# Kernel optimization log

Hardware: AMD Instinct MI355X
Metric: run time of the kernel (lower is better)

Reference implementation:

```python
import jax, jax.numpy as jnp
import numpy as np

ENC, TAG, LANG, ATT = 512, 512, 512, 256
N, P = 1024, 1024


def setup_inputs() -> dict:
    key = jax.random.key(0)
    ks = jax.random.split(key, 11)
    s = lambda d: 1.0 / np.sqrt(d)
    return {
        "encoder_out": jax.random.normal(ks[0], (1, P, ENC), jnp.float32),
        "decoder_hidden": jax.random.normal(ks[1], (N, TAG), jnp.float32),
        "language_out": jax.random.normal(ks[2], (N, LANG), jnp.float32),
        "We": jax.random.uniform(ks[3], (ATT, ENC), jnp.float32, -s(ENC), s(ENC)),
        "be": jax.random.uniform(ks[4], (ATT,), jnp.float32, -s(ENC), s(ENC)),
        "Wt": jax.random.uniform(ks[5], (ATT, TAG), jnp.float32, -s(TAG), s(TAG)),
        "bt": jax.random.uniform(ks[6], (ATT,), jnp.float32, -s(TAG), s(TAG)),
        "Wl": jax.random.uniform(ks[7], (ATT, LANG), jnp.float32, -s(LANG), s(LANG)),
        "bl": jax.random.uniform(ks[8], (ATT,), jnp.float32, -s(LANG), s(LANG)),
        "Wf": jax.random.uniform(ks[9], (1, ATT), jnp.float32, -s(ATT), s(ATT)),
        "bf": jax.random.uniform(ks[10], (1,), jnp.float32, -s(ATT), s(ATT)),
    }


def reference(encoder_out, decoder_hidden, language_out, We, be, Wt, bt, Wl, bl, Wf, bf):
    # att1: (1, P, A); att2, att3: (N, A)
    att1 = jnp.einsum("bpe,ae->bpa", encoder_out, We) + be
    att2 = decoder_hidden @ Wt.T + bt
    att3 = language_out @ Wl.T + bl
    # broadcast add -> (N, P, A), relu, reduce to scalar score per pixel
    h = jax.nn.relu(att1 + (att2 + att3)[:, None, :])  # (N, P, A)
    att = jnp.einsum("npa,a->np", h, Wf[0]) + bf[0]     # (N, P)
    alpha = jax.nn.softmax(att, axis=1)
    # softmax-weighted sum over pixels -> (N, ENC)
    awe = jnp.einsum("np,pe->ne", alpha, encoder_out[0])
    return awe, alpha
```

## Files before the change

### kernel.cpp

```cpp
#include <hip/hip_runtime.h>
#include <math.h>

#define ENC 512
#define ATT 256
#define NN 1024
#define PP 1024

typedef __attribute__((ext_vector_type(8))) __bf16 bf16x8;
typedef __attribute__((ext_vector_type(4))) float floatx4;
typedef __attribute__((ext_vector_type(2))) float floatx2;

union LdsVec { uint4 u; bf16x8 v; };

__device__ __forceinline__ unsigned short f2bf(float f) {
    union { float f; unsigned u; } x; x.f = f;
    unsigned r = x.u + 0x7fffu + ((x.u >> 16) & 1u);
    return (unsigned short)(r >> 16);
}

__device__ __forceinline__ int tile_off(int row, int k) {
    return row * 32 + ((((k >> 3) ^ ((row >> 1) & 3)) & 3) << 3) + (k & 7);
}

__device__ __forceinline__ void cvt_store(unsigned short* dst, int off, float4 f0, float4 f1) {
    unsigned short tmp[8] = {f2bf(f0.x), f2bf(f0.y), f2bf(f0.z), f2bf(f0.w),
                             f2bf(f1.x), f2bf(f1.y), f2bf(f1.z), f2bf(f1.w)};
    *(uint4*)&dst[off] = *(uint4*)tmp;
}

__global__ __launch_bounds__(256) void mfma_uv(
    const float* __restrict__ E,  const float* __restrict__ We, const float* __restrict__ be,
    const float* __restrict__ D,  const float* __restrict__ Wt, const float* __restrict__ bt,
    const float* __restrict__ Lg, const float* __restrict__ Wl, const float* __restrict__ bl,
    float* __restrict__ u, float* __restrict__ v1, float* __restrict__ v2)
{
    __shared__ __align__(16) unsigned short As[2][64 * 32];
    __shared__ __align__(16) unsigned short Bs[2][64 * 32];
    const int tid = threadIdx.x;
    const int K = 512;

    const float *A, *B, *bias; float* out;
    if      (blockIdx.z == 0) { A = E;  B = We; bias = be; out = u;  }
    else if (blockIdx.z == 1) { A = D;  B = Wt; bias = bt; out = v1; }
    else                      { A = Lg; B = Wl; bias = bl; out = v2; }

    const int m0 = blockIdx.y * 64, n0 = blockIdx.x * 64;
    const int wv = tid >> 6, lm = tid & 15, lq = (tid >> 4) & 3;
    const int mb = (wv & 1) * 32, nb = (wv >> 1) * 32;
    const int a0o = tile_off(mb + lm,      lq * 8);
    const int a1o = tile_off(mb + 16 + lm, lq * 8);
    const int b0o = tile_off(nb + lm,      lq * 8);
    const int b1o = tile_off(nb + 16 + lm, lq * 8);

    const int row = tid >> 2, kseg = tid & 3;
    const int soff = tile_off(row, kseg * 8);
    const float* Ap = A + (size_t)(m0 + row) * K + kseg * 8;
    const float* Bp = B + (size_t)(n0 + row) * K + kseg * 8;

    floatx4 acc[2][2];
    const floatx4 zero = {0.f, 0.f, 0.f, 0.f};
    acc[0][0] = zero; acc[0][1] = zero; acc[1][0] = zero; acc[1][1] = zero;

    float4 pa0 = *(const float4*)(Ap),     pa1 = *(const float4*)(Ap + 4);
    float4 pb0 = *(const float4*)(Bp),     pb1 = *(const float4*)(Bp + 4);

    for (int k0 = 0; k0 < K; k0 += 32) {
        const int buf = (k0 >> 5) & 1;
        cvt_store(As[buf], soff, pa0, pa1);
        cvt_store(Bs[buf], soff, pb0, pb1);
        __syncthreads();
        if (k0 + 32 < K) {
            pa0 = *(const float4*)(Ap + k0 + 32); pa1 = *(const float4*)(Ap + k0 + 36);
            pb0 = *(const float4*)(Bp + k0 + 32); pb1 = *(const float4*)(Bp + k0 + 36);
        }
        LdsVec fa0, fa1, fb0, fb1;
        fa0.u = *(const uint4*)&As[buf][a0o];
        fa1.u = *(const uint4*)&As[buf][a1o];
        fb0.u = *(const uint4*)&Bs[buf][b0o];
        fb1.u = *(const uint4*)&Bs[buf][b1o];
        acc[0][0] = __builtin_amdgcn_mfma_f32_16x16x32_bf16(fa0.v, fb0.v, acc[0][0], 0, 0, 0);
        acc[0][1] = __builtin_amdgcn_mfma_f32_16x16x32_bf16(fa0.v, fb1.v, acc[0][1], 0, 0, 0);
        acc[1][0] = __builtin_amdgcn_mfma_f32_16x16x32_bf16(fa1.v, fb0.v, acc[1][0], 0, 0, 0);
        acc[1][1] = __builtin_amdgcn_mfma_f32_16x16x32_bf16(fa1.v, fb1.v, acc[1][1], 0, 0, 0);
    }

    #pragma unroll
    for (int s = 0; s < 2; ++s) {
        const int col = n0 + nb + s * 16 + lm;
        const float bsum = bias[col];
        #pragma unroll
        for (int t = 0; t < 2; ++t)
            #pragma unroll
            for (int r = 0; r < 4; ++r)
                out[(size_t)(m0 + mb + t * 16 + lq * 4 + r) * ATT + col] = acc[t][s][r] + bsum;
    }
}

__global__ __launch_bounds__(256) void mfma_awe(
    const float* __restrict__ alpha, const float* __restrict__ Emat,
    float* __restrict__ awe)
{
    __shared__ __align__(16) unsigned short As[2][64 * 32];
    __shared__ __align__(16) unsigned short Bs[2][64 * 32];
    const int tid = threadIdx.x;
    const int K = PP;
    const int m0 = blockIdx.y * 64, n0 = blockIdx.x * 64;
    const int wv = tid >> 6, lm = tid & 15, lq = (tid >> 4) & 3;
    const int mb = (wv & 1) * 32, nb = (wv >> 1) * 32;
    const int a0o = tile_off(mb + lm,      lq * 8);
    const int a1o = tile_off(mb + 16 + lm, lq * 8);
    const int b0o = tile_off(nb + lm,      lq * 8);
    const int b1o = tile_off(nb + 16 + lm, lq * 8);

    const int row = tid >> 2, kseg = tid & 3;
    const int soff = tile_off(row, kseg * 8);
    const float* Ap = alpha + (size_t)(m0 + row) * K + kseg * 8;
    const int kr = tid >> 3, cc = (tid & 7) * 4;
    const float* Ep = Emat + (size_t)kr * ENC + n0;

    floatx4 acc[2][2];
    const floatx4 zero = {0.f, 0.f, 0.f, 0.f};
    acc[0][0] = zero; acc[0][1] = zero; acc[1][0] = zero; acc[1][1] = zero;

    float4 pa0 = *(const float4*)(Ap),  pa1 = *(const float4*)(Ap + 4);
    float4 pe0 = *(const float4*)(Ep + cc);
    float4 pe1 = *(const float4*)(Ep + cc + 32);

    for (int k0 = 0; k0 < K; k0 += 32) {
        const int buf = (k0 >> 5) & 1;
        cvt_store(As[buf], soff, pa0, pa1);
        unsigned short* Bb = Bs[buf];
        Bb[tile_off(cc + 0, kr)] = f2bf(pe0.x);
        Bb[tile_off(cc + 1, kr)] = f2bf(pe0.y);
        Bb[tile_off(cc + 2, kr)] = f2bf(pe0.z);
        Bb[tile_off(cc + 3, kr)] = f2bf(pe0.w);
        Bb[tile_off(cc + 32, kr)] = f2bf(pe1.x);
        Bb[tile_off(cc + 33, kr)] = f2bf(pe1.y);
        Bb[tile_off(cc + 34, kr)] = f2bf(pe1.z);
        Bb[tile_off(cc + 35, kr)] = f2bf(pe1.w);
        __syncthreads();
        if (k0 + 32 < K) {
            pa0 = *(const float4*)(Ap + k0 + 32); pa1 = *(const float4*)(Ap + k0 + 36);
            const float* ep = Ep + (size_t)(k0 + 32) * ENC;
            pe0 = *(const float4*)(ep + cc);
            pe1 = *(const float4*)(ep + cc + 32);
        }
        LdsVec fa0, fa1, fb0, fb1;
        fa0.u = *(const uint4*)&As[buf][a0o];
        fa1.u = *(const uint4*)&As[buf][a1o];
        fb0.u = *(const uint4*)&Bs[buf][b0o];
        fb1.u = *(const uint4*)&Bs[buf][b1o];
        acc[0][0] = __builtin_amdgcn_mfma_f32_16x16x32_bf16(fa0.v, fb0.v, acc[0][0], 0, 0, 0);
        acc[0][1] = __builtin_amdgcn_mfma_f32_16x16x32_bf16(fa0.v, fb1.v, acc[0][1], 0, 0, 0);
        acc[1][0] = __builtin_amdgcn_mfma_f32_16x16x32_bf16(fa1.v, fb0.v, acc[1][0], 0, 0, 0);
        acc[1][1] = __builtin_amdgcn_mfma_f32_16x16x32_bf16(fa1.v, fb1.v, acc[1][1], 0, 0, 0);
    }

    #pragma unroll
    for (int s = 0; s < 2; ++s) {
        const int col = n0 + nb + s * 16 + lm;
        #pragma unroll
        for (int t = 0; t < 2; ++t)
            #pragma unroll
            for (int r = 0; r < 4; ++r)
                awe[(size_t)(m0 + mb + t * 16 + lq * 4 + r) * ENC + col] = acc[t][s][r];
    }
}

__global__ __launch_bounds__(256) void att_fused(
    const float* __restrict__ u, const float* __restrict__ v1,
    const float* __restrict__ v2,
    const float* __restrict__ Wf, float* __restrict__ att)
{
    __shared__ float us[32][68];
    __shared__ float vs[32][36];
    __shared__ float wfs[ATT];
    const int tid = threadIdx.x;
    wfs[tid] = Wf[tid];
    const int p0 = blockIdx.x * 64, n0 = blockIdx.y * 32;
    const int urow = tid & 63, uas = tid >> 6;
    const int vrow = tid & 31, vas = tid >> 5;
    const int tx = tid & 15, ty = tid >> 4;

    floatx2 acc[2][2];
    const floatx2 z2 = {0.f, 0.f};
    acc[0][0] = z2; acc[0][1] = z2; acc[1][0] = z2; acc[1][1] = z2;

    for (int ac = 0; ac < ATT; ac += 32) {
        __syncthreads();
        {
            const float* up = &u[(size_t)(p0 + urow) * ATT + ac + uas * 8];
            float4 f0 = *(const float4*)up;
            float4 f1 = *(const float4*)(up + 4);
            us[uas*8+0][urow] = f0.x; us[uas*8+1][urow] = f0.y;
            us[uas*8+2][urow] = f0.z; us[uas*8+3][urow] = f0.w;
            us[uas*8+4][urow] = f1.x; us[uas*8+5][urow] = f1.y;
            us[uas*8+6][urow] = f1.z; us[uas*8+7][urow] = f1.w;
            const size_t vidx = (size_t)(n0 + vrow) * ATT + ac + vas * 4;
            float4 g  = *(const float4*)&v1[vidx];
            float4 g2 = *(const float4*)&v2[vidx];
            vs[vas*4+0][vrow] = g.x + g2.x; vs[vas*4+1][vrow] = g.y + g2.y;
            vs[vas*4+2][vrow] = g.z + g2.z; vs[vas*4+3][vrow] = g.w + g2.w;
        }
        __syncthreads();
        #pragma unroll
        for (int a = 0; a < 32; ++a) {
            float4 up4 = *(const float4*)&us[a][tx * 4];
            float2 vn2 = *(const float2*)&vs[a][ty * 2];
            const float w = wfs[ac + a];
            floatx2 u_lo = {up4.x, up4.y}, u_hi = {up4.z, up4.w};
            #pragma unroll
            for (int j = 0; j < 2; ++j) {
                const float vj = j ? vn2.y : vn2.x;
                floatx2 t0 = u_lo + vj;
                floatx2 t1 = u_hi + vj;
                t0.x = fmaxf(t0.x, 0.f); t0.y = fmaxf(t0.y, 0.f);
                t1.x = fmaxf(t1.x, 0.f); t1.y = fmaxf(t1.y, 0.f);
                acc[j][0] = t0 * w + acc[j][0];
                acc[j][1] = t1 * w + acc[j][1];
            }
        }
    }

    #pragma unroll
    for (int j = 0; j < 2; ++j) {
        float4 o;
        o.x = acc[j][0].x; o.y = acc[j][0].y; o.z = acc[j][1].x; o.w = acc[j][1].y;
        *(float4*)&att[(size_t)(n0 + ty * 2 + j) * PP + p0 + tx * 4] = o;
    }
}

__global__ __launch_bounds__(256) void softmax_rows(float* __restrict__ att)
{
    const int wv = threadIdx.x >> 6, lane = threadIdx.x & 63;
    const int n = blockIdx.x * 4 + wv;
    float* row = att + (size_t)n * PP;

    float4 x[4];
    #pragma unroll
    for (int i = 0; i < 4; ++i) x[i] = *(const float4*)&row[i * 256 + lane * 4];

    float m = -1e30f;
    #pragma unroll
    for (int i = 0; i < 4; ++i)
        m = fmaxf(m, fmaxf(fmaxf(x[i].x, x[i].y), fmaxf(x[i].z, x[i].w)));
    #pragma unroll
    for (int off = 32; off > 0; off >>= 1) m = fmaxf(m, __shfl_xor(m, off, 64));

    float s = 0.f;
    #pragma unroll
    for (int i = 0; i < 4; ++i) {
        x[i].x = __expf(x[i].x - m); x[i].y = __expf(x[i].y - m);
        x[i].z = __expf(x[i].z - m); x[i].w = __expf(x[i].w - m);
        s += x[i].x + x[i].y + x[i].z + x[i].w;
    }
    #pragma unroll
    for (int off = 32; off > 0; off >>= 1) s += __shfl_xor(s, off, 64);
    const float inv = 1.0f / s;

    #pragma unroll
    for (int i = 0; i < 4; ++i) {
        x[i].x *= inv; x[i].y *= inv; x[i].z *= inv; x[i].w *= inv;
        *(float4*)&row[i * 256 + lane * 4] = x[i];
    }
}

extern "C" void kernel_launch(void* const* d_in, const int* in_sizes, int n_in,
                              void* d_out, int out_size, void* d_ws, size_t ws_size,
                              hipStream_t stream)
{
    const float* encoder = (const float*)d_in[0];
    const float* dec     = (const float*)d_in[1];
    const float* lang    = (const float*)d_in[2];
    const float* We      = (const float*)d_in[3];
    const float* be      = (const float*)d_in[4];
    const float* Wt      = (const float*)d_in[5];
    const float* bt      = (const float*)d_in[6];
    const float* Wl      = (const float*)d_in[7];
    const float* bl      = (const float*)d_in[8];
    const float* Wf      = (const float*)d_in[9];

    float* u  = (float*)d_ws;
    float* v1 = u  + NN * ATT;
    float* v2 = v1 + NN * ATT;

    float* awe   = (float*)d_out;
    float* alpha = (float*)d_out + NN * ENC;

    mfma_uv<<<dim3(ATT / 64, NN / 64, 3), 256, 0, stream>>>(
        encoder, We, be, dec, Wt, bt, lang, Wl, bl, u, v1, v2);
    att_fused<<<dim3(PP / 64, NN / 32), 256, 0, stream>>>(u, v1, v2, Wf, alpha);
    softmax_rows<<<dim3(NN / 4), 256, 0, stream>>>(alpha);
    mfma_awe<<<dim3(ENC / 64, NN / 64), 256, 0, stream>>>(alpha, encoder, awe);
}
```

Measured before the change: 139.1 us.

## Transpose projections, split attention over ATT halves, pre-transpose encoder to bf16

The projection GEMM now writes u, v1, v2 transposed (ATT-major), so the attention kernel loads tiles with vectorized float4 copies instead of scalar transposing LDS stores. The attention kernel uses 64x64 tiles with 4 rows per thread and splits the ATT reduction across two z-slices that write partial scores. Softmax sums the partials and also emits a bf16 copy of alpha. An extra block slice transposes the encoder into bf16, so the awe GEMM streams bf16 operands with vector loads. This costs extra workspace traffic for the partial-score buffers and adds a second rounding path, with bf16 conversion moved to packed intrinsics.

```diff
diff --git a/kernel.cpp b/kernel.cpp
--- a/kernel.cpp
+++ b/kernel.cpp
@@ -1,4 +1,5 @@
 #include <hip/hip_runtime.h>
+#include <hip/hip_bf16.h>
 #include <math.h>
 
 #define ENC 512
@@ -12,37 +13,74 @@
 
 union LdsVec { uint4 u; bf16x8 v; };
 
-__device__ __forceinline__ unsigned short f2bf(float f) {
-    union { float f; unsigned u; } x; x.f = f;
-    unsigned r = x.u + 0x7fffu + ((x.u >> 16) & 1u);
-    return (unsigned short)(r >> 16);
+__device__ __forceinline__ unsigned cvt_pk(float lo, float hi) {
+    union { __hip_bfloat162 h; unsigned u; } x;
+    x.h = __float22bfloat162_rn(float2{lo, hi});
+    return x.u;
+}
+__device__ __forceinline__ uint4 cvt8(float4 f0, float4 f1) {
+    uint4 r;
+    r.x = cvt_pk(f0.x, f0.y); r.y = cvt_pk(f0.z, f0.w);
+    r.z = cvt_pk(f1.x, f1.y); r.w = cvt_pk(f1.z, f1.w);
+    return r;
 }
 
 __device__ __forceinline__ int tile_off(int row, int k) {
     return row * 32 + ((((k >> 3) ^ ((row >> 1) & 3)) & 3) << 3) + (k & 7);
 }
 
-__device__ __forceinline__ void cvt_store(unsigned short* dst, int off, float4 f0, float4 f1) {
-    unsigned short tmp[8] = {f2bf(f0.x), f2bf(f0.y), f2bf(f0.z), f2bf(f0.w),
-                             f2bf(f1.x), f2bf(f1.y), f2bf(f1.z), f2bf(f1.w)};
-    *(uint4*)&dst[off] = *(uint4*)tmp;
+__device__ __forceinline__ void stage_bt(unsigned short* dst, const float* __restrict__ src,
+                                         int ld, int k0, int tid) {
+    const int row = tid >> 2, kseg = tid & 3;
+    const float* p = src + (size_t)row * ld + k0 + kseg * 8;
+    float4 f0 = *(const float4*)p;
+    float4 f1 = *(const float4*)(p + 4);
+    uint4 u = cvt8(f0, f1);
+    *(uint4*)&dst[tile_off(row, kseg * 8)] = u;
 }
 
 __global__ __launch_bounds__(256) void mfma_uv(
     const float* __restrict__ E,  const float* __restrict__ We, const float* __restrict__ be,
     const float* __restrict__ D,  const float* __restrict__ Wt, const float* __restrict__ bt,
     const float* __restrict__ Lg, const float* __restrict__ Wl, const float* __restrict__ bl,
-    float* __restrict__ u, float* __restrict__ v1, float* __restrict__ v2)
-{
+    float* __restrict__ uT, float* __restrict__ v1T, float* __restrict__ v2T,
+    unsigned short* __restrict__ ET)
+{
+    const int tid = threadIdx.x;
+
+    if (blockIdx.z == 3) {
+        __shared__ unsigned short T[64][72];
+        const int k0 = blockIdx.y * 64;
+        const int kr = tid >> 2, nc = (tid & 3) * 16;
+        const int nr = tid >> 2, kc = (tid & 3) * 16;
+        #pragma unroll
+        for (int t = 0; t < 2; ++t) {
+            const int n0 = (blockIdx.x * 2 + t) * 64;
+            const float* ep = E + (size_t)(k0 + kr) * ENC + n0 + nc;
+            float4 a = *(const float4*)(ep + 0),  b = *(const float4*)(ep + 4);
+            float4 c = *(const float4*)(ep + 8),  d = *(const float4*)(ep + 12);
+            if (t) __syncthreads();
+            *(uint4*)&T[kr][nc]     = cvt8(a, b);
+            *(uint4*)&T[kr][nc + 8] = cvt8(c, d);
+            __syncthreads();
+            unsigned short tmp[16];
+            #pragma unroll
+            for (int i = 0; i < 16; ++i) tmp[i] = T[kc + i][nr];
+            unsigned short* op = ET + (size_t)(n0 + nr) * PP + k0 + kc;
+            *(uint4*)(op)     = *(uint4*)&tmp[0];
+            *(uint4*)(op + 8) = *(uint4*)&tmp[8];
+        }
+        return;
+    }
+
     __shared__ __align__(16) unsigned short As[2][64 * 32];
     __shared__ __align__(16) unsigned short Bs[2][64 * 32];
-    const int tid = threadIdx.x;
     const int K = 512;
 
     const float *A, *B, *bias; float* out;
-    if      (blockIdx.z == 0) { A = E;  B = We; bias = be; out = u;  }
-    else if (blockIdx.z == 1) { A = D;  B = Wt; bias = bt; out = v1; }
-    else                      { A = Lg; B = Wl; bias = bl; out = v2; }
+    if      (blockIdx.z == 0) { A = E;  B = We; bias = be; out = uT;  }
+    else if (blockIdx.z == 1) { A = D;  B = Wt; bias = bt; out = v1T; }
+    else                      { A = Lg; B = Wl; bias = bl; out = v2T; }
 
     const int m0 = blockIdx.y * 64, n0 = blockIdx.x * 64;
     const int wv = tid >> 6, lm = tid & 15, lq = (tid >> 4) & 3;
@@ -61,13 +99,13 @@
     const floatx4 zero = {0.f, 0.f, 0.f, 0.f};
     acc[0][0] = zero; acc[0][1] = zero; acc[1][0] = zero; acc[1][1] = zero;
 
-    float4 pa0 = *(const float4*)(Ap),     pa1 = *(const float4*)(Ap + 4);
-    float4 pb0 = *(const float4*)(Bp),     pb1 = *(const float4*)(Bp + 4);
+    float4 pa0 = *(const float4*)(Ap), pa1 = *(const float4*)(Ap + 4);
+    float4 pb0 = *(const float4*)(Bp), pb1 = *(const float4*)(Bp + 4);
 
     for (int k0 = 0; k0 < K; k0 += 32) {
         const int buf = (k0 >> 5) & 1;
-        cvt_store(As[buf], soff, pa0, pa1);
-        cvt_store(Bs[buf], soff, pb0, pb1);
+        *(uint4*)&As[buf][soff] = cvt8(pa0, pa1);
+        *(uint4*)&Bs[buf][soff] = cvt8(pb0, pb1);
         __syncthreads();
         if (k0 + 32 < K) {
             pa0 = *(const float4*)(Ap + k0 + 32); pa1 = *(const float4*)(Ap + k0 + 36);
@@ -89,156 +127,106 @@
         const int col = n0 + nb + s * 16 + lm;
         const float bsum = bias[col];
         #pragma unroll
-        for (int t = 0; t < 2; ++t)
-            #pragma unroll
-            for (int r = 0; r < 4; ++r)
-                out[(size_t)(m0 + mb + t * 16 + lq * 4 + r) * ATT + col] = acc[t][s][r] + bsum;
-    }
-}
-
-__global__ __launch_bounds__(256) void mfma_awe(
-    const float* __restrict__ alpha, const float* __restrict__ Emat,
-    float* __restrict__ awe)
-{
-    __shared__ __align__(16) unsigned short As[2][64 * 32];
-    __shared__ __align__(16) unsigned short Bs[2][64 * 32];
+        for (int t = 0; t < 2; ++t) {
+            const int mbase = m0 + mb + t * 16 + lq * 4;
+            float4 o;
+            o.x = acc[t][s][0] + bsum; o.y = acc[t][s][1] + bsum;
+            o.z = acc[t][s][2] + bsum; o.w = acc[t][s][3] + bsum;
+            *(float4*)&out[(size_t)col * NN + mbase] = o;
+        }
+    }
+}
+
+__global__ __launch_bounds__(256) void att_fused(
+    const float* __restrict__ uT, const float* __restrict__ v1T,
+    const float* __restrict__ v2T,
+    const float* __restrict__ Wf, float* __restrict__ att_part)
+{
+    __shared__ float us[32][68];
+    __shared__ float vs[32][68];
+    __shared__ float wfs[128];
     const int tid = threadIdx.x;
-    const int K = PP;
-    const int m0 = blockIdx.y * 64, n0 = blockIdx.x * 64;
-    const int wv = tid >> 6, lm = tid & 15, lq = (tid >> 4) & 3;
-    const int mb = (wv & 1) * 32, nb = (wv >> 1) * 32;
-    const int a0o = tile_off(mb + lm,      lq * 8);
-    const int a1o = tile_off(mb + 16 + lm, lq * 8);
-    const int b0o = tile_off(nb + lm,      lq * 8);
-    const int b1o = tile_off(nb + 16 + lm, lq * 8);
-
-    const int row = tid >> 2, kseg = tid & 3;
-    const int soff = tile_off(row, kseg * 8);
-    const float* Ap = alpha + (size_t)(m0 + row) * K + kseg * 8;
-    const int kr = tid >> 3, cc = (tid & 7) * 4;
-    const float* Ep = Emat + (size_t)kr * ENC + n0;
-
-    floatx4 acc[2][2];
-    const floatx4 zero = {0.f, 0.f, 0.f, 0.f};
-    acc[0][0] = zero; acc[0][1] = zero; acc[1][0] = zero; acc[1][1] = zero;
-
-    float4 pa0 = *(const float4*)(Ap),  pa1 = *(const float4*)(Ap + 4);
-    float4 pe0 = *(const float4*)(Ep + cc);
-    float4 pe1 = *(const float4*)(Ep + cc + 32);
-
-    for (int k0 = 0; k0 < K; k0 += 32) {
-        const int buf = (k0 >> 5) & 1;
-        cvt_store(As[buf], soff, pa0, pa1);
-        unsigned short* Bb = Bs[buf];
-        Bb[tile_off(cc + 0, kr)] = f2bf(pe0.x);
-        Bb[tile_off(cc + 1, kr)] = f2bf(pe0.y);
-        Bb[tile_off(cc + 2, kr)] = f2bf(pe0.z);
-        Bb[tile_off(cc + 3, kr)] = f2bf(pe0.w);
-        Bb[tile_off(cc + 32, kr)] = f2bf(pe1.x);
-        Bb[tile_off(cc + 33, kr)] = f2bf(pe1.y);
-        Bb[tile_off(cc + 34, kr)] = f2bf(pe1.z);
-        Bb[tile_off(cc + 35, kr)] = f2bf(pe1.w);
-        __syncthreads();
-        if (k0 + 32 < K) {
-            pa0 = *(const float4*)(Ap + k0 + 32); pa1 = *(const float4*)(Ap + k0 + 36);
-            const float* ep = Ep + (size_t)(k0 + 32) * ENC;
-            pe0 = *(const float4*)(ep + cc);
-            pe1 = *(const float4*)(ep + cc + 32);
-        }
-        LdsVec fa0, fa1, fb0, fb1;
-        fa0.u = *(const uint4*)&As[buf][a0o];
-        fa1.u = *(const uint4*)&As[buf][a1o];
-        fb0.u = *(const uint4*)&Bs[buf][b0o];
-        fb1.u = *(const uint4*)&Bs[buf][b1o];
-        acc[0][0] = __builtin_amdgcn_mfma_f32_16x16x32_bf16(fa0.v, fb0.v, acc[0][0], 0, 0, 0);
-        acc[0][1] = __builtin_amdgcn_mfma_f32_16x16x32_bf16(fa0.v, fb1.v, acc[0][1], 0, 0, 0);
-        acc[1][0] = __builtin_amdgcn_mfma_f32_16x16x32_bf16(fa1.v, fb0.v, acc[1][0], 0, 0, 0);
-        acc[1][1] = __builtin_amdgcn_mfma_f32_16x16x32_bf16(fa1.v, fb1.v, acc[1][1], 0, 0, 0);
-    }
-
-    #pragma unroll
-    for (int s = 0; s < 2; ++s) {
-        const int col = n0 + nb + s * 16 + lm;
-        #pragma unroll
-        for (int t = 0; t < 2; ++t)
-            #pragma unroll
-            for (int r = 0; r < 4; ++r)
-                awe[(size_t)(m0 + mb + t * 16 + lq * 4 + r) * ENC + col] = acc[t][s][r];
-    }
-}
-
-__global__ __launch_bounds__(256) void att_fused(
-    const float* __restrict__ u, const float* __restrict__ v1,
-    const float* __restrict__ v2,
-    const float* __restrict__ Wf, float* __restrict__ att)
-{
-    __shared__ float us[32][68];
-    __shared__ float vs[32][36];
-    __shared__ float wfs[ATT];
-    const int tid = threadIdx.x;
-    wfs[tid] = Wf[tid];
-    const int p0 = blockIdx.x * 64, n0 = blockIdx.y * 32;
-    const int urow = tid & 63, uas = tid >> 6;
-    const int vrow = tid & 31, vas = tid >> 5;
+    const int z = blockIdx.z;
+    if (tid < 128) wfs[tid] = Wf[z * 128 + tid];
+    const int p0 = blockIdx.x * 64, n0 = blockIdx.y * 64;
+    const int rowS = tid >> 3, cS = (tid & 7) * 8;
     const int tx = tid & 15, ty = tid >> 4;
 
-    floatx2 acc[2][2];
+    floatx2 acc[4][2];
     const floatx2 z2 = {0.f, 0.f};
-    acc[0][0] = z2; acc[0][1] = z2; acc[1][0] = z2; acc[1][1] = z2;
-
-    for (int ac = 0; ac < ATT; ac += 32) {
+    #pragma unroll
+    for (int j = 0; j < 4; ++j) { acc[j][0] = z2; acc[j][1] = z2; }
+
+    const int abase = z * 128;
+    for (int ac = 0; ac < 128; ac += 32) {
         __syncthreads();
         {
-            const float* up = &u[(size_t)(p0 + urow) * ATT + ac + uas * 8];
+            const float* up = &uT[(size_t)(abase + ac + rowS) * NN + p0 + cS];
             float4 f0 = *(const float4*)up;
             float4 f1 = *(const float4*)(up + 4);
-            us[uas*8+0][urow] = f0.x; us[uas*8+1][urow] = f0.y;
-            us[uas*8+2][urow] = f0.z; us[uas*8+3][urow] = f0.w;
-            us[uas*8+4][urow] = f1.x; us[uas*8+5][urow] = f1.y;
-            us[uas*8+6][urow] = f1.z; us[uas*8+7][urow] = f1.w;
-            const size_t vidx = (size_t)(n0 + vrow) * ATT + ac + vas * 4;
-            float4 g  = *(const float4*)&v1[vidx];
-            float4 g2 = *(const float4*)&v2[vidx];
-            vs[vas*4+0][vrow] = g.x + g2.x; vs[vas*4+1][vrow] = g.y + g2.y;
-            vs[vas*4+2][vrow] = g.z + g2.z; vs[vas*4+3][vrow] = g.w + g2.w;
+            *(float4*)&us[rowS][cS]     = f0;
+            *(float4*)&us[rowS][cS + 4] = f1;
+            const size_t vidx = (size_t)(abase + ac + rowS) * NN + n0 + cS;
+            float4 g0 = *(const float4*)&v1T[vidx];
+            float4 g1 = *(const float4*)&v1T[vidx + 4];
+            float4 h0 = *(const float4*)&v2T[vidx];
+            float4 h1 = *(const float4*)&v2T[vidx + 4];
+            float4 s0, s1;
+            s0.x = g0.x + h0.x; s0.y = g0.y + h0.y; s0.z = g0.z + h0.z; s0.w = g0.w + h0.w;
+            s1.x = g1.x + h1.x; s1.y = g1.y + h1.y; s1.z = g1.z + h1.z; s1.w = g1.w + h1.w;
+            *(float4*)&vs[rowS][cS]     = s0;
+            *(float4*)&vs[rowS][cS + 4] = s1;
         }
         __syncthreads();
         #pragma unroll
-        for (int a = 0; a < 32; ++a) {
-            float4 up4 = *(const float4*)&us[a][tx * 4];
-            float2 vn2 = *(const float2*)&vs[a][ty * 2];
-            const float w = wfs[ac + a];
-            floatx2 u_lo = {up4.x, up4.y}, u_hi = {up4.z, up4.w};
+        for (int a4 = 0; a4 < 32; a4 += 4) {
+            float4 w4 = *(const float4*)&wfs[ac + a4];
             #pragma unroll
-            for (int j = 0; j < 2; ++j) {
-                const float vj = j ? vn2.y : vn2.x;
-                floatx2 t0 = u_lo + vj;
-                floatx2 t1 = u_hi + vj;
-                t0.x = fmaxf(t0.x, 0.f); t0.y = fmaxf(t0.y, 0.f);
-                t1.x = fmaxf(t1.x, 0.f); t1.y = fmaxf(t1.y, 0.f);
-                acc[j][0] = t0 * w + acc[j][0];
-                acc[j][1] = t1 * w + acc[j][1];
+            for (int aa = 0; aa < 4; ++aa) {
+                const int a = a4 + aa;
+                float4 u4 = *(const float4*)&us[a][tx * 4];
+                float4 v4 = *(const float4*)&vs[a][ty * 4];
+                const float w = (aa == 0) ? w4.x : (aa == 1) ? w4.y : (aa == 2) ? w4.z : w4.w;
+                floatx2 ulo = {u4.x, u4.y}, uhi = {u4.z, u4.w};
+                const float vv[4] = {v4.x, v4.y, v4.z, v4.w};
+                #pragma unroll
+                for (int j = 0; j < 4; ++j) {
+                    floatx2 t0 = ulo + vv[j];
+                    floatx2 t1 = uhi + vv[j];
+                    t0 = __builtin_elementwise_max(t0, z2);
+                    t1 = __builtin_elementwise_max(t1, z2);
+                    acc[j][0] = t0 * w + acc[j][0];
+                    acc[j][1] = t1 * w + acc[j][1];
+                }
             }
         }
     }
 
-    #pragma unroll
-    for (int j = 0; j < 2; ++j) {
+    float* outp = att_part + (size_t)z * NN * PP;
+    #pragma unroll
+    for (int j = 0; j < 4; ++j) {
         float4 o;
         o.x = acc[j][0].x; o.y = acc[j][0].y; o.z = acc[j][1].x; o.w = acc[j][1].y;
-        *(float4*)&att[(size_t)(n0 + ty * 2 + j) * PP + p0 + tx * 4] = o;
-    }
-}
-
-__global__ __launch_bounds__(256) void softmax_rows(float* __restrict__ att)
+        *(float4*)&outp[(size_t)(n0 + ty * 4 + j) * PP + p0 + tx * 4] = o;
+    }
+}
+
+__global__ __launch_bounds__(256) void softmax_rows(
+    const float* __restrict__ att_part, float* __restrict__ alpha,
+    unsigned short* __restrict__ alpha_bf)
 {
     const int wv = threadIdx.x >> 6, lane = threadIdx.x & 63;
     const int n = blockIdx.x * 4 + wv;
-    float* row = att + (size_t)n * PP;
+    const float* r0 = att_part + (size_t)n * PP;
+    const float* r1 = att_part + (size_t)NN * PP + (size_t)n * PP;
 
     float4 x[4];
     #pragma unroll
-    for (int i = 0; i < 4; ++i) x[i] = *(const float4*)&row[i * 256 + lane * 4];
+    for (int i = 0; i < 4; ++i) {
+        float4 a = *(const float4*)&r0[i * 256 + lane * 4];
+        float4 b = *(const float4*)&r1[i * 256 + lane * 4];
+        x[i].x = a.x + b.x; x[i].y = a.y + b.y; x[i].z = a.z + b.z; x[i].w = a.w + b.w;
+    }
 
     float m = -1e30f;
     #pragma unroll
@@ -258,10 +246,71 @@
     for (int off = 32; off > 0; off >>= 1) s += __shfl_xor(s, off, 64);
     const float inv = 1.0f / s;
 
+    float* ar = alpha + (size_t)n * PP;
+    unsigned short* br = alpha_bf + (size_t)n * PP;
     #pragma unroll
     for (int i = 0; i < 4; ++i) {
         x[i].x *= inv; x[i].y *= inv; x[i].z *= inv; x[i].w *= inv;
-        *(float4*)&row[i * 256 + lane * 4] = x[i];
+        *(float4*)&ar[i * 256 + lane * 4] = x[i];
+        uint2 pk;
+        pk.x = cvt_pk(x[i].x, x[i].y);
+        pk.y = cvt_pk(x[i].z, x[i].w);
+        *(uint2*)&br[i * 256 + lane * 4] = pk;
+    }
+}
+
+__global__ __launch_bounds__(256) void mfma_awe(
+    const unsigned short* __restrict__ alpha_bf,
+    const unsigned short* __restrict__ ET, float* __restrict__ awe)
+{
+    __shared__ __align__(16) unsigned short As[2][32 * 32];
+    __shared__ __align__(16) unsigned short Bs[2][64 * 32];
+    const int tid = threadIdx.x;
+    const int K = PP;
+    const int m0 = blockIdx.y * 32, n0 = blockIdx.x * 64;
+    const int wv = tid >> 6, lm = tid & 15, lq = (tid >> 4) & 3;
+    const int mw = (wv & 1) * 16, nw = (wv >> 1) * 32;
+    const int a0o = tile_off(mw + lm,      lq * 8);
+    const int b0o = tile_off(nw + lm,      lq * 8);
+    const int b1o = tile_off(nw + 16 + lm, lq * 8);
+
+    const int rowA = tid >> 3, kcA = (tid & 7) * 4;
+    const int rowB = tid >> 2, kcB = (tid & 3) * 8;
+    const int aoff = tile_off(rowA, kcA);
+    const int boff = tile_off(rowB, kcB);
+    const unsigned short* Ap = alpha_bf + (size_t)(m0 + rowA) * PP + kcA;
+    const unsigned short* Bp = ET + (size_t)(n0 + rowB) * PP + kcB;
+
+    floatx4 acc[2];
+    const floatx4 zero = {0.f, 0.f, 0.f, 0.f};
+    acc[0] = zero; acc[1] = zero;
+
+    uint2 pa = *(const uint2*)Ap;
+    uint4 pb = *(const uint4*)Bp;
+
+    for (int k0 = 0; k0 < K; k0 += 32) {
+        const int buf = (k0 >> 5) & 1;
+        *(uint2*)&As[buf][aoff] = pa;
+        *(uint4*)&Bs[buf][boff] = pb;
+        __syncthreads();
+        if (k0 + 32 < K) {
+            pa = *(const uint2*)(Ap + k0 + 32);
+            pb = *(const uint4*)(Bp + k0 + 32);
+        }
+        LdsVec fa, fb0, fb1;
+        fa.u  = *(const uint4*)&As[buf][a0o];
+        fb0.u = *(const uint4*)&Bs[buf][b0o];
+        fb1.u = *(const uint4*)&Bs[buf][b1o];
+        acc[0] = __builtin_amdgcn_mfma_f32_16x16x32_bf16(fa.v, fb0.v, acc[0], 0, 0, 0);
+        acc[1] = __builtin_amdgcn_mfma_f32_16x16x32_bf16(fa.v, fb1.v, acc[1], 0, 0, 0);
+    }
+
+    #pragma unroll
+    for (int s = 0; s < 2; ++s) {
+        const int col = n0 + nw + s * 16 + lm;
+        #pragma unroll
+        for (int r = 0; r < 4; ++r)
+            awe[(size_t)(m0 + mw + lq * 4 + r) * ENC + col] = acc[s][r];
     }
 }
 
@@ -280,16 +329,19 @@
     const float* bl      = (const float*)d_in[8];
     const float* Wf      = (const float*)d_in[9];
 
-    float* u  = (float*)d_ws;
-    float* v1 = u  + NN * ATT;
-    float* v2 = v1 + NN * ATT;
+    float* uT   = (float*)d_ws;
+    float* v1T  = uT  + ATT * NN;
+    float* v2T  = v1T + ATT * NN;
+    float* attp = v2T + ATT * NN;
+    unsigned short* alpha_bf = (unsigned short*)(attp + 2 * (size_t)NN * PP);
+    unsigned short* ET       = alpha_bf + (size_t)NN * PP;
 
     float* awe   = (float*)d_out;
     float* alpha = (float*)d_out + NN * ENC;
 
-    mfma_uv<<<dim3(ATT / 64, NN / 64, 3), 256, 0, stream>>>(
-        encoder, We, be, dec, Wt, bt, lang, Wl, bl, u, v1, v2);
-    att_fused<<<dim3(PP / 64, NN / 32), 256, 0, stream>>>(u, v1, v2, Wf, alpha);
-    softmax_rows<<<dim3(NN / 4), 256, 0, stream>>>(alpha);
-    mfma_awe<<<dim3(ENC / 64, NN / 64), 256, 0, stream>>>(alpha, encoder, awe);
-}
+    mfma_uv<<<dim3(4, 16, 4), 256, 0, stream>>>(
+        encoder, We, be, dec, Wt, bt, lang, Wl, bl, uT, v1T, v2T, ET);
+    att_fused<<<dim3(PP / 64, NN / 64, 2), 256, 0, stream>>>(uT, v1T, v2T, Wf, attp);
+    softmax_rows<<<dim3(NN / 4), 256, 0, stream>>>(attp, alpha, alpha_bf);
+    mfma_awe<<<dim3(ENC / 64, NN / 32), 256, 0, stream>>>(alpha_bf, ET, awe);
+}
```

After: 126.1 us, median of 2. 9.4% less time.
